# Performance work log

Measured on AMD Instinct MI355X. Metric: run time of the kernel, lower is better.

Reference implementation:

```python
import jax, jax.numpy as jnp
import numpy as np

N_HEADS = 32
N_KV_HEADS = 8
HEAD_DIM = 128
N_REP = N_HEADS // N_KV_HEADS
Q_SIZE = N_HEADS * HEAD_DIM        # 4096
K_SIZE = N_KV_HEADS * HEAD_DIM     # 1024


def setup_inputs() -> dict:
    key = jax.random.key(0)
    ks = jax.random.split(key, 5)
    B, T, D = 2, 2048, 4096
    x = jax.random.normal(ks[0], (B, T, D), dtype=jnp.float32)
    # complex freqs_cis split into real (cos) and imag (sin) parts, [T, head_dim/2]
    pos = jnp.arange(T, dtype=jnp.float32)[:, None]
    inv_freq = 1.0 / (10000.0 ** (jnp.arange(0, HEAD_DIM, 2, dtype=jnp.float32) / HEAD_DIM))
    ang = pos * inv_freq[None, :]
    freqs_cos = jnp.cos(ang)
    freqs_sin = jnp.sin(ang)
    w_qkv = jax.random.normal(ks[1], (Q_SIZE + 2 * K_SIZE, D), dtype=jnp.float32) * (D ** -0.5)
    wo_w = jax.random.normal(ks[2], (D, Q_SIZE), dtype=jnp.float32) * (Q_SIZE ** -0.5)
    return {"x": x, "freqs_cos": freqs_cos, "freqs_sin": freqs_sin, "w_qkv": w_qkv, "wo_w": wo_w}


def _apply_rotary(t, cos, sin):
    # t: [B, T, H, D]; cos/sin: [T, D/2] -> broadcast to [1, T, 1, D/2]
    tr = t.reshape(t.shape[:-1] + (HEAD_DIM // 2, 2))
    t0, t1 = tr[..., 0], tr[..., 1]
    c = cos[None, :, None, :]
    s = sin[None, :, None, :]
    o0 = t0 * c - t1 * s
    o1 = t0 * s + t1 * c
    return jnp.stack([o0, o1], axis=-1).reshape(t.shape)


def reference(x, freqs_cos, freqs_sin, w_qkv, wo_w):
    B, T, _ = x.shape
    qkv = jnp.einsum('btd,nd->btn', x, w_qkv)  # fused QKV GEMM
    q = qkv[..., :Q_SIZE].reshape(B, T, N_HEADS, HEAD_DIM)
    k = qkv[..., Q_SIZE:Q_SIZE + K_SIZE].reshape(B, T, N_KV_HEADS, HEAD_DIM)
    v = qkv[..., Q_SIZE + K_SIZE:].reshape(B, T, N_KV_HEADS, HEAD_DIM)
    q = _apply_rotary(q, freqs_cos, freqs_sin)
    k = _apply_rotary(k, freqs_cos, freqs_sin)
    # [B, H, T, D]
    q = q.transpose(0, 2, 1, 3)
    k = k.transpose(0, 2, 1, 3)
    v = v.transpose(0, 2, 1, 3)
    # GQA repeat_interleave along head dim
    k = jnp.repeat(k, N_REP, axis=1)
    v = jnp.repeat(v, N_REP, axis=1)
    scale = HEAD_DIM ** -0.5
    scores = jnp.einsum('bhqd,bhkd->bhqk', q, k) * scale
    causal = jnp.tril(jnp.ones((T, T), dtype=bool))
    scores = jnp.where(causal[None, None], scores, jnp.finfo(scores.dtype).min)
    attn = jax.nn.softmax(scores, axis=-1)
    y = jnp.einsum('bhqk,bhkd->bhqd', attn, v)
    y = y.transpose(0, 2, 1, 3).reshape(B, T, Q_SIZE)
    return jnp.einsum('btn,dn->btd', y, wo_w)
```

## Files before the change

kernel.cpp:

```cpp
#include <hip/hip_runtime.h>

typedef unsigned short u16t;
typedef unsigned int   u32t;
typedef __attribute__((ext_vector_type(8))) __bf16          bf16x8;
typedef __attribute__((ext_vector_type(8))) unsigned short  u16x8;
typedef __attribute__((ext_vector_type(4))) unsigned short  u16x4;
typedef __attribute__((ext_vector_type(4))) float           floatx4;

__device__ __forceinline__ u16t f2b(float f){
  u32t u = __builtin_bit_cast(u32t, f);
  u += 0x7fffu + ((u >> 16) & 1u);
  return (u16t)(u >> 16);
}
__device__ __forceinline__ float b2f(u16t h){
  return __builtin_bit_cast(float, (u32t)h << 16);
}
__device__ __forceinline__ void async16(const void* g, void* l){
  __builtin_amdgcn_global_load_lds((__attribute__((address_space(1))) void*)g,
                                   (__attribute__((address_space(3))) void*)l, 16, 0, 0);
}
__device__ __forceinline__ bf16x8 ldfrag(const u16t* p){
  return __builtin_bit_cast(bf16x8, *(const u16x8*)p);
}

__global__ __launch_bounds__(256)
void cvt_f32_bf16(const float* __restrict__ in, u16t* __restrict__ out, int n4){
  typedef __attribute__((ext_vector_type(4))) float f32x4;
  const f32x4* in4 = (const f32x4*)in;
  int stride = gridDim.x * blockDim.x;
  for (int i = blockIdx.x * blockDim.x + threadIdx.x; i < n4; i += stride){
    f32x4 v = in4[i];
    u16x4 o; o[0]=f2b(v[0]); o[1]=f2b(v[1]); o[2]=f2b(v[2]); o[3]=f2b(v[3]);
    *(u16x4*)(out + (size_t)i * 4) = o;
  }
}

#define MFMA16 __builtin_amdgcn_mfma_f32_16x16x32_bf16
template<int OUT_BF16>
__global__ __launch_bounds__(512, 2)
void gemm256(const u16t* __restrict__ A, const u16t* __restrict__ B,
             void* __restrict__ Cv, int M, int N, int K)
{
  (void)M;
  __shared__ u16t smem[65536];
  const int tid  = threadIdx.x;
  const int w    = tid >> 6, lane = tid & 63;
  const int lrow = lane & 15, quad = lane >> 4;
  const int wr   = w >> 2,  wc = w & 3;

  const int nwg  = (int)(gridDim.x * gridDim.y);
  const int flat = (int)(blockIdx.y * gridDim.x + blockIdx.x);
  const int q8 = nwg >> 3, r8 = nwg & 7, xcd = flat & 7, idx = flat >> 3;
  const int wg = (xcd < r8 ? xcd * (q8 + 1) : r8 * (q8 + 1) + (xcd - r8) * q8) + idx;
  const int m0 = (wg / (int)gridDim.x) * 256;
  const int n0 = (wg % (int)gridDim.x) * 256;

  const int srow = lane >> 3;
  const int scol = ((lane & 7) ^ srow) * 8;
  const u16t* gA = A + (size_t)(m0 + w * 8 + srow) * K + scol;
  const u16t* gB = B + (size_t)(n0 + w * 8 + srow) * K + scol;
  char* const ldsA = (char*)smem + w * 1024;
  char* const ldsB = (char*)smem + 65536 + w * 1024;
#define STA(h, i, buf, kt) async16(gA + (size_t)((h)*128 + (i)*64) * K + (kt)*64, \
                                   ldsA + (buf)*32768 + ((h)*2+(i))*8192)
#define STB(h, i, buf, kt) async16(gB + (size_t)((h)*128 + (i)*64) * K + (kt)*64, \
                                   ldsB + (buf)*32768 + ((h)*2+(i))*8192)

  const char* const sbb = (const char*)smem;
  const int c0   = ((quad ^ (lrow & 7)) * 16);
  const int aoff = (wr * 128 + lrow) * 128;
  const int boff = 65536 + (wc * 64 + lrow) * 128;

  floatx4 acc[8][4] = {};
  bf16x8 A0f[4][2], A1f[4][2], Bf0[2][2], Bf1[2][2];
  const int NT = K >> 6;

  STA(0,0,0,0); STA(0,1,0,0); STA(1,0,0,0); STA(1,1,0,0);
  STB(0,0,0,0); STB(0,1,0,0); STB(1,0,0,0); STB(1,1,0,0);
  STA(0,0,1,1); STA(0,1,1,1); STA(1,0,1,1); STA(1,1,1,1);
  STB(0,0,1,1); STB(0,1,1,1);
  asm volatile("s_waitcnt vmcnt(6)" ::: "memory");
  __builtin_amdgcn_sched_barrier(0);
  __builtin_amdgcn_s_barrier();

  for (int t = 0; t < NT; ++t){
    const int bsel = t & 1, nb = bsel ^ 1;
    const int bo = bsel * 32768;

#pragma unroll
    for (int mi = 0; mi < 4; ++mi){
      A0f[mi][0] = ldfrag((const u16t*)(sbb + bo + aoff + mi * 2048 + c0));
      A0f[mi][1] = ldfrag((const u16t*)(sbb + bo + aoff + mi * 2048 + (c0 ^ 64)));
    }
#pragma unroll
    for (int ni = 0; ni < 2; ++ni){
      Bf0[ni][0] = ldfrag((const u16t*)(sbb + bo + boff + ni * 2048 + c0));
      Bf0[ni][1] = ldfrag((const u16t*)(sbb + bo + boff + ni * 2048 + (c0 ^ 64)));
    }
    if (t + 1 < NT){ STB(1,0,nb,t+1); STB(1,1,nb,t+1); }
    __builtin_amdgcn_s_barrier();
    asm volatile("s_waitcnt lgkmcnt(0)" ::: "memory");
    __builtin_amdgcn_sched_barrier(0);
    __builtin_amdgcn_s_setprio(1);
#pragma unroll
    for (int mi = 0; mi < 4; ++mi)
#pragma unroll
      for (int ni = 0; ni < 2; ++ni){
        acc[mi][ni] = MFMA16(A0f[mi][0], Bf0[ni][0], acc[mi][ni], 0, 0, 0);
        acc[mi][ni] = MFMA16(A0f[mi][1], Bf0[ni][1], acc[mi][ni], 0, 0, 0);
      }
    __builtin_amdgcn_s_setprio(0);
    __builtin_amdgcn_sched_barrier(0);
    __builtin_amdgcn_s_barrier();

#pragma unroll
    for (int mi = 0; mi < 4; ++mi){
      A1f[mi][0] = ldfrag((const u16t*)(sbb + bo + aoff + (4 + mi) * 2048 + c0));
      A1f[mi][1] = ldfrag((const u16t*)(sbb + bo + aoff + (4 + mi) * 2048 + (c0 ^ 64)));
    }
    if (t + 2 < NT){ STA(0,0,bsel,t+2); STA(0,1,bsel,t+2); }
    __builtin_amdgcn_s_barrier();
    asm volatile("s_waitcnt lgkmcnt(0)" ::: "memory");
    __builtin_amdgcn_sched_barrier(0);
    __builtin_amdgcn_s_setprio(1);
#pragma unroll
    for (int mi = 0; mi < 4; ++mi)
#pragma unroll
      for (int ni = 0; ni < 2; ++ni){
        acc[4+mi][ni] = MFMA16(A1f[mi][0], Bf0[ni][0], acc[4+mi][ni], 0, 0, 0);
        acc[4+mi][ni] = MFMA16(A1f[mi][1], Bf0[ni][1], acc[4+mi][ni], 0, 0, 0);
      }
    __builtin_amdgcn_s_setprio(0);
    __builtin_amdgcn_sched_barrier(0);
    __builtin_amdgcn_s_barrier();

#pragma unroll
    for (int ni = 0; ni < 2; ++ni){
      Bf1[ni][0] = ldfrag((const u16t*)(sbb + bo + boff + (2 + ni) * 2048 + c0));
      Bf1[ni][1] = ldfrag((const u16t*)(sbb + bo + boff + (2 + ni) * 2048 + (c0 ^ 64)));
    }
    if (t + 2 < NT){ STA(1,0,bsel,t+2); STA(1,1,bsel,t+2); }
    __builtin_amdgcn_s_barrier();
    asm volatile("s_waitcnt lgkmcnt(0)" ::: "memory");
    __builtin_amdgcn_sched_barrier(0);
    __builtin_amdgcn_s_setprio(1);
#pragma unroll
    for (int mi = 0; mi < 4; ++mi)
#pragma unroll
      for (int ni = 0; ni < 2; ++ni){
        acc[mi][2+ni] = MFMA16(A0f[mi][0], Bf1[ni][0], acc[mi][2+ni], 0, 0, 0);
        acc[mi][2+ni] = MFMA16(A0f[mi][1], Bf1[ni][1], acc[mi][2+ni], 0, 0, 0);
      }
    __builtin_amdgcn_s_setprio(0);
    __builtin_amdgcn_sched_barrier(0);
    __builtin_amdgcn_s_barrier();

    if (t + 2 < NT){ STB(0,0,bsel,t+2); STB(0,1,bsel,t+2); }
    __builtin_amdgcn_s_barrier();
    __builtin_amdgcn_s_setprio(1);
#pragma unroll
    for (int mi = 0; mi < 4; ++mi)
#pragma unroll
      for (int ni = 0; ni < 2; ++ni){
        acc[4+mi][2+ni] = MFMA16(A1f[mi][0], Bf1[ni][0], acc[4+mi][2+ni], 0, 0, 0);
        acc[4+mi][2+ni] = MFMA16(A1f[mi][1], Bf1[ni][1], acc[4+mi][2+ni], 0, 0, 0);
      }
    __builtin_amdgcn_s_setprio(0);
    __builtin_amdgcn_sched_barrier(0);
    if (t + 2 < NT) asm volatile("s_waitcnt vmcnt(6)" ::: "memory");
    else            asm volatile("s_waitcnt vmcnt(0)" ::: "memory");
    __builtin_amdgcn_sched_barrier(0);
    __builtin_amdgcn_s_barrier();
  }

#pragma unroll
  for (int mi = 0; mi < 8; ++mi)
#pragma unroll
    for (int ni = 0; ni < 4; ++ni)
#pragma unroll
      for (int r = 0; r < 4; ++r){
        int row = m0 + wr * 128 + mi * 16 + quad * 4 + r;
        int col = n0 + wc * 64 + ni * 16 + lrow;
        float v = acc[mi][ni][r];
        if (OUT_BF16) ((u16t*)Cv)[(size_t)row * N + col] = f2b(v);
        else          ((float*)Cv)[(size_t)row * N + col] = v;
      }
#undef STA
#undef STB
}

__global__ __launch_bounds__(256)
void rope_qk(const u16t* __restrict__ qkvb, const float* __restrict__ cosp,
             const float* __restrict__ sinp, u16t* __restrict__ qr, u16t* __restrict__ kr)
{
  const int row = blockIdx.x;
  const int b = row >> 11, t = row & 2047;
  const u16t* src = qkvb + (size_t)row * 6144;
  for (int p = threadIdx.x; p < 2560; p += 256){
    u32t both = *(const u32t*)(src + 2 * p);
    float t0 = b2f((u16t)(both & 0xffff));
    float t1 = b2f((u16t)(both >> 16));
    int j = p & 63;
    float c = cosp[t * 64 + j], s = sinp[t * 64 + j];
    float o0 = t0 * c - t1 * s;
    float o1 = t0 * s + t1 * c;
    u32t packed = (u32t)f2b(o0) | ((u32t)f2b(o1) << 16);
    if (p < 2048){
      int h = p >> 6;
      *(u32t*)(qr + (((size_t)(b * 32 + h) * 2048 + t) * 128 + 2 * j)) = packed;
    } else {
      int kh = (p - 2048) >> 6;
      *(u32t*)(kr + (((size_t)(b * 8 + kh) * 2048 + t) * 128 + 2 * j)) = packed;
    }
  }
}

__global__ __launch_bounds__(256)
void vtrans(const u16t* __restrict__ qkvb, u16t* __restrict__ vt)
{
  __shared__ u16t sV[64 * 128];
  const int tid = threadIdx.x;
  const int blk = blockIdx.x;
  const int tile = blk & 31, kvh = (blk >> 5) & 7, b = blk >> 8;
  const int t0 = tile * 64;
  const size_t srcbase = (size_t)(b * 2048 + t0) * 6144 + 5120 + kvh * 128;
#pragma unroll
  for (int it = 0; it < 4; ++it){
    int task = it * 256 + tid;
    int rrow = task >> 4, cb = task & 15;
    *(u16x8*)&sV[rrow * 128 + cb * 8] =
        *(const u16x8*)(qkvb + srcbase + (size_t)rrow * 6144 + cb * 8);
  }
  __syncthreads();
  const size_t dstbase = (size_t)((b * 8 + kvh) * 128) * 2048 + t0;
#pragma unroll
  for (int it = 0; it < 4; ++it){
    int task = it * 256 + tid;
    int tc = task & 7, d = task >> 3;
    u16x8 v;
#pragma unroll
    for (int j = 0; j < 8; ++j) v[j] = sV[(tc * 8 + j) * 128 + d];
    *(u16x8*)(vt + dstbase + (size_t)d * 2048 + tc * 8) = v;
  }
}

__global__ __launch_bounds__(256)
void attn_fwd(const u16t* __restrict__ Qg, const u16t* __restrict__ Kg,
              const u16t* __restrict__ Vt, u16t* __restrict__ Y)
{
  __shared__ u16t smem[25600];
  u16t* sK = smem;
  u16t* sV = smem + 8192;
  u16t* sP = smem + 16384;

  const int tid  = threadIdx.x;
  const int wave = tid >> 6, lane = tid & 63;
  const int lrow = lane & 15, quad = lane >> 4;
  const int qt = 15 - (int)blockIdx.y;
  const int q0 = qt * 128;
  const int bh = blockIdx.x;
  const int b = bh >> 5, h = bh & 31, kvh = h >> 2;
  const float qscale = 0.088388347648318447f * 1.4426950408889634f;

  bf16x8 aq[2][4];
  const size_t qbase = ((size_t)bh * 2048 + q0 + wave * 32) * 128;
#pragma unroll
  for (int qs = 0; qs < 2; ++qs)
#pragma unroll
    for (int kk = 0; kk < 4; ++kk)
      aq[qs][kk] = ldfrag(Qg + qbase + (size_t)(qs * 16 + lrow) * 128 + (kk * 4 + quad) * 8);

  float mi[2][4], li[2][4];
#pragma unroll
  for (int qs = 0; qs < 2; ++qs)
#pragma unroll
    for (int r = 0; r < 4; ++r){ mi[qs][r] = -1e30f; li[qs][r] = 0.f; }
  floatx4 o[2][8] = {};
  const size_t kbase = ((size_t)(b * 8 + kvh) * 2048) * 128;
  const size_t vbase = ((size_t)(b * 8 + kvh) * 128) * 2048;
  const int ktiles = 2 * qt + 2;

  for (int kt = 0; kt < ktiles; ++kt){
    const int k0 = kt * 64;
#pragma unroll
    for (int r = 0; r < 4; ++r){
      const int dc = r * 4 + wave;
      async16(Kg + kbase + (size_t)(k0 + lane) * 128 + dc * 8, (char*)sK + dc * 1024);
    }
#pragma unroll
    for (int r = 0; r < 4; ++r){
      const int kvc = r * 2 + (wave >> 1);
      const int dd  = (wave & 1) * 64 + lane;
      async16(Vt + vbase + (size_t)dd * 2048 + k0 + kvc * 8,
              (char*)sV + kvc * 2048 + (wave & 1) * 1024);
    }
    __syncthreads();

    floatx4 s[2][4] = {};
#pragma unroll
    for (int kk = 0; kk < 4; ++kk){
#pragma unroll
      for (int nt = 0; nt < 4; ++nt){
        bf16x8 bk = ldfrag(&sK[((kk * 4 + quad) * 64 + nt * 16 + lrow) * 8]);
        s[0][nt] = __builtin_amdgcn_mfma_f32_16x16x32_bf16(aq[0][kk], bk, s[0][nt], 0, 0, 0);
        s[1][nt] = __builtin_amdgcn_mfma_f32_16x16x32_bf16(aq[1][kk], bk, s[1][nt], 0, 0, 0);
      }
    }

#pragma unroll
    for (int qs = 0; qs < 2; ++qs){
      float tt[4][4];
#pragma unroll
      for (int nt = 0; nt < 4; ++nt)
#pragma unroll
        for (int r = 0; r < 4; ++r)
          tt[nt][r] = s[qs][nt][r] * qscale;
      const int qrb = q0 + wave * 32 + qs * 16 + quad * 4;
      if (kt >= ktiles - 2){
#pragma unroll
        for (int nt = 0; nt < 4; ++nt){
          int kc = k0 + nt * 16 + lrow;
#pragma unroll
          for (int r = 0; r < 4; ++r)
            if (kc > qrb + r) tt[nt][r] = -1e30f;
        }
      }
      float rmax[4];
#pragma unroll
      for (int r = 0; r < 4; ++r)
        rmax[r] = fmaxf(fmaxf(tt[0][r], tt[1][r]), fmaxf(tt[2][r], tt[3][r]));
#pragma unroll
      for (int off = 1; off < 16; off <<= 1){
#pragma unroll
        for (int r = 0; r < 4; ++r)
          rmax[r] = fmaxf(rmax[r], __shfl_xor(rmax[r], off, 64));
      }
      float alpha[4];
#pragma unroll
      for (int r = 0; r < 4; ++r){
        float mn = fmaxf(mi[qs][r], rmax[r]);
        alpha[r] = __builtin_amdgcn_exp2f(mi[qs][r] - mn);
        mi[qs][r] = mn;
      }
      float lsum[4] = {0.f, 0.f, 0.f, 0.f};
#pragma unroll
      for (int nt = 0; nt < 4; ++nt)
#pragma unroll
        for (int r = 0; r < 4; ++r){
          float e = __builtin_amdgcn_exp2f(tt[nt][r] - mi[qs][r]);
          lsum[r] += e;
          sP[(wave * 32 + qs * 16 + quad * 4 + r) * 72 + nt * 16 + lrow] = f2b(e);
        }
#pragma unroll
      for (int off = 1; off < 16; off <<= 1){
#pragma unroll
        for (int r = 0; r < 4; ++r)
          lsum[r] += __shfl_xor(lsum[r], off, 64);
      }
#pragma unroll
      for (int r = 0; r < 4; ++r) li[qs][r] = li[qs][r] * alpha[r] + lsum[r];
#pragma unroll
      for (int nt = 0; nt < 8; ++nt){
        o[qs][nt][0] *= alpha[0]; o[qs][nt][1] *= alpha[1];
        o[qs][nt][2] *= alpha[2]; o[qs][nt][3] *= alpha[3];
      }
    }

#pragma unroll
    for (int kk = 0; kk < 2; ++kk){
      bf16x8 ap0 = ldfrag(&sP[(wave * 32 + lrow) * 72 + kk * 32 + quad * 8]);
      bf16x8 ap1 = ldfrag(&sP[(wave * 32 + 16 + lrow) * 72 + kk * 32 + quad * 8]);
#pragma unroll
      for (int nt = 0; nt < 8; ++nt){
        bf16x8 bv = ldfrag(&sV[((kk * 4 + quad) * 128 + nt * 16 + lrow) * 8]);
        o[0][nt] = __builtin_amdgcn_mfma_f32_16x16x32_bf16(ap0, bv, o[0][nt], 0, 0, 0);
        o[1][nt] = __builtin_amdgcn_mfma_f32_16x16x32_bf16(ap1, bv, o[1][nt], 0, 0, 0);
      }
    }
    __syncthreads();
  }

#pragma unroll
  for (int qs = 0; qs < 2; ++qs)
#pragma unroll
    for (int r = 0; r < 4; ++r){
      int t = q0 + wave * 32 + qs * 16 + quad * 4 + r;
      float inv = 1.0f / li[qs][r];
      size_t ybase = ((size_t)(b * 2048 + t)) * 4096 + h * 128;
#pragma unroll
      for (int nt = 0; nt < 8; ++nt)
        Y[ybase + nt * 16 + lrow] = f2b(o[qs][nt][r] * inv);
    }
}

extern "C" void kernel_launch(void* const* d_in, const int* in_sizes, int n_in,
                              void* d_out, int out_size, void* d_ws, size_t ws_size,
                              hipStream_t stream)
{
  (void)in_sizes; (void)n_in; (void)out_size; (void)ws_size;
  const float* x    = (const float*)d_in[0];
  const float* fc   = (const float*)d_in[1];
  const float* fs   = (const float*)d_in[2];
  const float* wqkv = (const float*)d_in[3];
  const float* wo   = (const float*)d_in[4];
  float* out = (float*)d_out;

  char* ws = (char*)d_ws;
  u16t* xb    = (u16t*)(ws);
  u16t* wqkvb = (u16t*)(ws + 33554432);
  u16t* wob   = (u16t*)(ws + 83886080);
  u16t* qkvb  = (u16t*)(ws + 117440512);
  u16t* qr    = (u16t*)(ws + 167772160);
  u16t* kr    = (u16t*)(ws + 201326592);
  u16t* vt    = (u16t*)(ws + 209715200);
  u16t* yb    = xb;

  cvt_f32_bf16<<<4096, 256, 0, stream>>>(x,    xb,    16777216 / 4);
  cvt_f32_bf16<<<4096, 256, 0, stream>>>(wqkv, wqkvb, 25165824 / 4);
  cvt_f32_bf16<<<4096, 256, 0, stream>>>(wo,   wob,   16777216 / 4);
  gemm256<1><<<dim3(24, 16), 512, 0, stream>>>(xb, wqkvb, qkvb, 4096, 6144, 4096);
  rope_qk<<<4096, 256, 0, stream>>>(qkvb, fc, fs, qr, kr);
  vtrans<<<512, 256, 0, stream>>>(qkvb, vt);
  attn_fwd<<<dim3(64, 16), 256, 0, stream>>>(qr, kr, vt, yb);
  gemm256<0><<<dim3(16, 16), 512, 0, stream>>>(yb, wob, out, 4096, 4096, 4096);
}
```

Baseline: 884.7 us.

## Double-buffer K tiles and overlap async loads with attention compute

K tiles are now double-buffered in LDS: the next K tile is prefetched while the current tile's QK^T and softmax run. The V load is issued at the top of each iteration and only waited on before the PV MFMAs, using explicit vmcnt waits and raw s_barrier in place of __syncthreads. s_setprio is raised around the MFMA blocks. This aims to hide global-to-LDS latency, at the cost of more LDS per block (lower occupancy) and fragile hand-counted waitcnt values.

```diff
diff --git a/kernel.cpp b/kernel.cpp
--- a/kernel.cpp
+++ b/kernel.cpp
@@ -248,10 +248,9 @@
 void attn_fwd(const u16t* __restrict__ Qg, const u16t* __restrict__ Kg,
               const u16t* __restrict__ Vt, u16t* __restrict__ Y)
 {
-  __shared__ u16t smem[25600];
-  u16t* sK = smem;
-  u16t* sV = smem + 8192;
-  u16t* sP = smem + 16384;
+  __shared__ u16t smem[33792];
+  u16t* sV = smem + 16384;
+  u16t* sP = smem + 24576;
 
   const int tid  = threadIdx.x;
   const int wave = tid >> 6, lane = tid & 63;
@@ -270,42 +269,65 @@
     for (int kk = 0; kk < 4; ++kk)
       aq[qs][kk] = ldfrag(Qg + qbase + (size_t)(qs * 16 + lrow) * 128 + (kk * 4 + quad) * 8);
 
+  const size_t kbase = ((size_t)(b * 8 + kvh) * 2048) * 128;
+  const size_t vbase = ((size_t)(b * 8 + kvh) * 128) * 2048;
+
+#define STAGEK(kt_, bs_) {                                                      \
+    const int k0_ = (kt_) * 64;                                                 \
+    char* dK = (char*)smem + (bs_) * 16384;                                     \
+    _Pragma("unroll")                                                           \
+    for (int r = 0; r < 4; ++r){                                                \
+      const int dc = r * 4 + wave;                                              \
+      async16(Kg + kbase + (size_t)(k0_ + lane) * 128 + dc * 8, dK + dc * 1024);\
+    } }
+#define STAGEV(kt_) {                                                           \
+    const int k0_ = (kt_) * 64;                                                 \
+    char* dV = (char*)smem + 32768;                                             \
+    _Pragma("unroll")                                                           \
+    for (int r = 0; r < 4; ++r){                                                \
+      const int kvc = r * 2 + (wave >> 1);                                      \
+      const int dd  = (wave & 1) * 64 + lane;                                   \
+      async16(Vt + vbase + (size_t)dd * 2048 + k0_ + kvc * 8,                   \
+              dV + kvc * 2048 + (wave & 1) * 1024);                             \
+    } }
+
   float mi[2][4], li[2][4];
 #pragma unroll
   for (int qs = 0; qs < 2; ++qs)
 #pragma unroll
     for (int r = 0; r < 4; ++r){ mi[qs][r] = -1e30f; li[qs][r] = 0.f; }
   floatx4 o[2][8] = {};
-  const size_t kbase = ((size_t)(b * 8 + kvh) * 2048) * 128;
-  const size_t vbase = ((size_t)(b * 8 + kvh) * 128) * 2048;
   const int ktiles = 2 * qt + 2;
 
+  STAGEK(0, 0);
+
   for (int kt = 0; kt < ktiles; ++kt){
+    const int bsel = kt & 1;
     const int k0 = kt * 64;
-#pragma unroll
-    for (int r = 0; r < 4; ++r){
-      const int dc = r * 4 + wave;
-      async16(Kg + kbase + (size_t)(k0 + lane) * 128 + dc * 8, (char*)sK + dc * 1024);
-    }
-#pragma unroll
-    for (int r = 0; r < 4; ++r){
-      const int kvc = r * 2 + (wave >> 1);
-      const int dd  = (wave & 1) * 64 + lane;
-      async16(Vt + vbase + (size_t)dd * 2048 + k0 + kvc * 8,
-              (char*)sV + kvc * 2048 + (wave & 1) * 1024);
-    }
-    __syncthreads();
+    STAGEV(kt);
+    if (kt + 1 < ktiles){
+      STAGEK(kt + 1, bsel ^ 1);
+      asm volatile("s_waitcnt vmcnt(8)" ::: "memory");
+    } else {
+      asm volatile("s_waitcnt vmcnt(4)" ::: "memory");
+    }
+    __builtin_amdgcn_sched_barrier(0);
+    __builtin_amdgcn_s_barrier();
+
+    const u16t* cK = smem + bsel * 8192;
 
     floatx4 s[2][4] = {};
+    __builtin_amdgcn_s_setprio(1);
 #pragma unroll
     for (int kk = 0; kk < 4; ++kk){
 #pragma unroll
       for (int nt = 0; nt < 4; ++nt){
-        bf16x8 bk = ldfrag(&sK[((kk * 4 + quad) * 64 + nt * 16 + lrow) * 8]);
+        bf16x8 bk = ldfrag(&cK[((kk * 4 + quad) * 64 + nt * 16 + lrow) * 8]);
         s[0][nt] = __builtin_amdgcn_mfma_f32_16x16x32_bf16(aq[0][kk], bk, s[0][nt], 0, 0, 0);
         s[1][nt] = __builtin_amdgcn_mfma_f32_16x16x32_bf16(aq[1][kk], bk, s[1][nt], 0, 0, 0);
       }
     }
+    __builtin_amdgcn_s_setprio(0);
 
 #pragma unroll
     for (int qs = 0; qs < 2; ++qs){
@@ -366,6 +388,12 @@
       }
     }
 
+    if (kt + 1 < ktiles) asm volatile("s_waitcnt vmcnt(4)" ::: "memory");
+    else                 asm volatile("s_waitcnt vmcnt(0)" ::: "memory");
+    __builtin_amdgcn_sched_barrier(0);
+    __builtin_amdgcn_s_barrier();
+
+    __builtin_amdgcn_s_setprio(1);
 #pragma unroll
     for (int kk = 0; kk < 2; ++kk){
       bf16x8 ap0 = ldfrag(&sP[(wave * 32 + lrow) * 72 + kk * 32 + quad * 8]);
@@ -377,8 +405,12 @@
         o[1][nt] = __builtin_amdgcn_mfma_f32_16x16x32_bf16(ap1, bv, o[1][nt], 0, 0, 0);
       }
     }
-    __syncthreads();
-  }
+    __builtin_amdgcn_s_setprio(0);
+    __builtin_amdgcn_sched_barrier(0);
+    __builtin_amdgcn_s_barrier();
+  }
+#undef STAGEK
+#undef STAGEV
 
 #pragma unroll
   for (int qs = 0; qs < 2; ++qs)
```

Result: faster. 834.3 us (-5.7%).
